# Optimization experiments

Measured on AMD Instinct MI355X. Metric: run time of the kernel, lower is better.

Reference implementation:

```python
import jax, jax.numpy as jnp
from jax import lax
import numpy as np

N, D, K = 262144, 256, 32


def setup_inputs() -> dict:
    key = jax.random.key(0)
    k1, k2 = jax.random.split(key)
    inputs = jax.random.normal(k1, (N, D), dtype=jnp.float32)
    q_vectors = jax.random.normal(k2, (K, D), dtype=jnp.float32)
    return {"inputs": inputs, "q_vectors": q_vectors}


def reference(inputs, q_vectors):
    # Sequence of Householder reflections: x <- x - (x @ q) outer (2/||q||^2 q)
    squared_norms = jnp.sum(q_vectors ** 2, axis=-1)  # [K]

    def step(x, qn):
        q, sq = qn  # q: [D], sq: scalar
        coeff = x @ q  # [N]
        x = x - jnp.outer(coeff, (2.0 / sq) * q)  # rank-1 update, [N, D]
        return x, None

    outputs, _ = lax.scan(step, inputs, (q_vectors, squared_norms))
    logabsdet = jnp.zeros(inputs.shape[0], dtype=inputs.dtype)
    return outputs, logabsdet
```

## Files before the change

kernel.cpp:

```cpp
#include <hip/hip_runtime.h>

#define N_ROWS 262144
#define DDIM   256
#define KREF   32
#define TILES  4
#define GRID_WY (N_ROWS / (64 * TILES))

typedef __attribute__((ext_vector_type(4))) float f32x4;
typedef __attribute__((ext_vector_type(8))) short bf16x8;

__device__ bf16x8 g_Vhi[2 * 8 * 64];
__device__ bf16x8 g_Vlo[2 * 8 * 64];
__device__ bf16x8 g_Uhi[16 * 64];
__device__ bf16x8 g_Ulo[16 * 64];
__device__ float  g_T[32 * 32];

__device__ __forceinline__ unsigned short f2bf(float x) {
    unsigned u = __float_as_uint(x);
    u += 0x7fffu + ((u >> 16) & 1u);
    return (unsigned short)(u >> 16);
}
__device__ __forceinline__ float bf2f(unsigned short h) {
    return __uint_as_float(((unsigned)h) << 16);
}

#define QS_LD 264
#define T_LD  33

__global__ __launch_bounds__(256)
void setup_a(const float* __restrict__ Q) {
    __shared__ float Qs[32 * QS_LD];
    __shared__ float G[32 * 32];
    __shared__ float T[32 * T_LD];
    __shared__ float beta[32];
    const int tid = threadIdx.x;

    {
        const int q  = tid >> 3;
        const int c8 = tid & 7;
        const f32x4* src = (const f32x4*)(Q + q * DDIM);
        f32x4* dst = (f32x4*)(Qs + q * QS_LD);
        #pragma unroll
        for (int i = 0; i < 8; ++i)
            dst[c8 + 8 * i] = src[c8 + 8 * i];
    }
    __syncthreads();

    for (int p = tid; p < 1024; p += 256) {
        const int i = p >> 5, j = p & 31;
        const f32x4* qi = (const f32x4*)(Qs + i * QS_LD);
        const f32x4* qj = (const f32x4*)(Qs + j * QS_LD);
        float s = 0.f;
        #pragma unroll 8
        for (int d = 0; d < 64; ++d) {
            const f32x4 a = qi[d], b = qj[d];
            s += a.x * b.x + a.y * b.y + a.z * b.z + a.w * b.w;
        }
        G[p] = s;
    }
    for (int p = tid; p < 32 * T_LD; p += 256) T[p] = 0.f;
    __syncthreads();

    if (tid < 32) beta[tid] = 2.0f / G[tid * 32 + tid];
    __syncthreads();

    for (int k = 0; k < 32; ++k) {
        if (tid < k) {
            float s = 0.f;
            for (int j = tid; j < k; ++j) s += T[tid * T_LD + j] * G[j * 32 + k];
            T[tid * T_LD + k] = -beta[k] * s;
        } else if (tid == k) {
            T[k * T_LD + k] = beta[k];
        }
        __syncthreads();
    }

    for (int p = tid; p < 1024; p += 256)
        g_T[p] = T[(p >> 5) * T_LD + (p & 31)];

    for (int e = tid; e < 2 * 8 * 64; e += 256) {
        const int lane = e & 63, c = (e >> 6) & 7, nt = e >> 9;
        const int q  = 16 * nt + (lane & 15);
        const int d0 = 32 * c + 8 * (lane >> 4);
        bf16x8 vh, vl;
        #pragma unroll
        for (int j = 0; j < 8; ++j) {
            const float x = Qs[q * QS_LD + d0 + j];
            const unsigned short h = f2bf(x);
            vh[j] = (short)h;
            vl[j] = (short)f2bf(x - bf2f(h));
        }
        g_Vhi[e] = vh; g_Vlo[e] = vl;
    }
}

__global__ __launch_bounds__(256)
void setup_b(const float* __restrict__ Q) {
    __shared__ float Ts[32 * 32];
    __shared__ float Us[16 * 33];
    const int tid = threadIdx.x;
    const int m = blockIdx.x;

    for (int p = tid; p < 1024; p += 256) Ts[p] = g_T[p];
    __syncthreads();

    #pragma unroll
    for (int e = 0; e < 2; ++e) {
        const int idx = tid + 256 * e;
        const int dd = idx >> 5, k = idx & 31;
        const int d = 16 * m + dd;
        float s = 0.f;
        for (int j = k; j < 32; ++j) s += Ts[k * 32 + j] * Q[j * DDIM + d];
        Us[dd * 33 + k] = s;
    }
    __syncthreads();

    if (tid < 64) {
        const int dd = tid & 15, k0 = 8 * (tid >> 4);
        bf16x8 uh, ul;
        #pragma unroll
        for (int j = 0; j < 8; ++j) {
            const float x = Us[dd * 33 + k0 + j];
            const unsigned short h = f2bf(x);
            uh[j] = (short)h;
            ul[j] = (short)f2bf(x - bf2f(h));
        }
        g_Uhi[m * 64 + tid] = uh;
        g_Ulo[m * 64 + tid] = ul;
    }
}

__global__ __launch_bounds__(256, 2)
void wy_kernel(const float* __restrict__ X, float* __restrict__ out) {
    __shared__ bf16x8 sVhi[1024];
    __shared__ bf16x8 sVlo[1024];
    __shared__ float  tscr[4 * 16 * 36];

    const int tid  = threadIdx.x;
    const int wave = tid >> 6;
    const int lane = tid & 63;
    const int t = lane & 15;
    const int g = lane >> 4;

    {
        const f32x4* s1 = (const f32x4*)g_Vhi;
        const f32x4* s2 = (const f32x4*)g_Vlo;
        f32x4* d1 = (f32x4*)sVhi;
        f32x4* d2 = (f32x4*)sVlo;
        #pragma unroll
        for (int i = 0; i < 4; ++i) {
            d1[tid + 256 * i] = s1[tid + 256 * i];
            d2[tid + 256 * i] = s2[tid + 256 * i];
        }
    }
    __syncthreads();

    const size_t base = (size_t)blockIdx.x * (64 * TILES) + wave * 16 + t;
    float* tb = tscr + wave * (16 * 36);

    f32x4 xa[16];
    {
        const float* xp = X + base * DDIM + 8 * g;
        #pragma unroll
        for (int c = 0; c < 8; ++c) {
            xa[2 * c]     = *(const f32x4*)(xp + 32 * c);
            xa[2 * c + 1] = *(const f32x4*)(xp + 32 * c + 4);
        }
    }

    #pragma unroll
    for (int tt = 0; tt < TILES; ++tt) {
        const size_t row = base + (size_t)tt * 64;

        bf16x8 ahi[8], alo[8];
        #pragma unroll
        for (int c = 0; c < 8; ++c) {
            #pragma unroll
            for (int e = 0; e < 8; ++e) {
                const float x = (e < 4) ? xa[2 * c][e] : xa[2 * c + 1][e - 4];
                const unsigned short h = f2bf(x);
                ahi[c][e] = (short)h;
                alo[c][e] = (short)f2bf(x - bf2f(h));
            }
        }

        if (tt + 1 < TILES) {
            const float* xp = X + (row + 64) * DDIM + 8 * g;
            #pragma unroll
            for (int c = 0; c < 8; ++c) {
                xa[2 * c]     = *(const f32x4*)(xp + 32 * c);
                xa[2 * c + 1] = *(const f32x4*)(xp + 32 * c + 4);
            }
        }

        f32x4 a0h = {0.f, 0.f, 0.f, 0.f}, a0l = {0.f, 0.f, 0.f, 0.f};
        f32x4 a1h = {0.f, 0.f, 0.f, 0.f}, a1l = {0.f, 0.f, 0.f, 0.f};
        #pragma unroll
        for (int c = 0; c < 8; ++c) {
            const bf16x8 bh0 = sVhi[c * 64 + lane];
            const bf16x8 bl0 = sVlo[c * 64 + lane];
            const bf16x8 bh1 = sVhi[512 + c * 64 + lane];
            const bf16x8 bl1 = sVlo[512 + c * 64 + lane];
            a0h = __builtin_amdgcn_mfma_f32_16x16x32_bf16(ahi[c], bh0, a0h, 0, 0, 0);
            a0l = __builtin_amdgcn_mfma_f32_16x16x32_bf16(alo[c], bh0, a0l, 0, 0, 0);
            a0l = __builtin_amdgcn_mfma_f32_16x16x32_bf16(ahi[c], bl0, a0l, 0, 0, 0);
            a1h = __builtin_amdgcn_mfma_f32_16x16x32_bf16(ahi[c], bh1, a1h, 0, 0, 0);
            a1l = __builtin_amdgcn_mfma_f32_16x16x32_bf16(alo[c], bh1, a1l, 0, 0, 0);
            a1l = __builtin_amdgcn_mfma_f32_16x16x32_bf16(ahi[c], bl1, a1l, 0, 0, 0);
        }
        const f32x4 acc0 = a0h + a0l;
        const f32x4 acc1 = a1h + a1l;

        f32x4 xe[16];
        const float* xr = X + row * DDIM + 4 * g;
        #pragma unroll
        for (int mt = 0; mt < 16; ++mt)
            xe[mt] = *(const f32x4*)(xr + 16 * mt);

        #pragma unroll
        for (int r = 0; r < 4; ++r) {
            tb[(4 * g + r) * 36 + t]      = acc0[r];
            tb[(4 * g + r) * 36 + 16 + t] = acc1[r];
        }
        asm volatile("s_waitcnt lgkmcnt(0)" ::: "memory");
        const f32x4 c01 = *(const f32x4*)(tb + t * 36 + 8 * g);
        const f32x4 c23 = *(const f32x4*)(tb + t * 36 + 8 * g + 4);

        bf16x8 chi, clo;
        #pragma unroll
        for (int j = 0; j < 8; ++j) {
            const float v = -((j < 4) ? c01[j] : c23[j - 4]);
            const unsigned short h = f2bf(v);
            chi[j] = (short)h;
            clo[j] = (short)f2bf(v - bf2f(h));
        }

        float* op = out + row * DDIM + 4 * g;
        #pragma unroll
        for (int mt = 0; mt < 16; ++mt) {
            const bf16x8 uh = g_Uhi[mt * 64 + lane];
            const bf16x8 ul = g_Ulo[mt * 64 + lane];
            f32x4 a = xe[mt];
            a = __builtin_amdgcn_mfma_f32_16x16x32_bf16(uh, chi, a, 0, 0, 0);
            a = __builtin_amdgcn_mfma_f32_16x16x32_bf16(ul, chi, a, 0, 0, 0);
            a = __builtin_amdgcn_mfma_f32_16x16x32_bf16(uh, clo, a, 0, 0, 0);
            *(f32x4*)(op + 16 * mt) = a;
        }
    }

    out[(size_t)N_ROWS * DDIM + (size_t)blockIdx.x * 256 + tid] = 0.0f;
}

extern "C" void kernel_launch(void* const* d_in, const int* in_sizes, int n_in,
                              void* d_out, int out_size, void* d_ws, size_t ws_size,
                              hipStream_t stream) {
    const float* X = (const float*)d_in[0];
    const float* Q = (const float*)d_in[1];
    float* out = (float*)d_out;

    setup_a<<<1, 256, 0, stream>>>(Q);
    setup_b<<<16, 256, 0, stream>>>(Q);
    wy_kernel<<<GRID_WY, 256, 0, stream>>>(X, out);
}
```

Before: 524.0 us.

## Process one 64-row tile per block instead of four with register prefetch

```diff
diff --git a/kernel.cpp b/kernel.cpp
--- a/kernel.cpp
+++ b/kernel.cpp
@@ -3,8 +3,7 @@
 #define N_ROWS 262144
 #define DDIM   256
 #define KREF   32
-#define TILES  4
-#define GRID_WY (N_ROWS / (64 * TILES))
+#define GRID_WY (N_ROWS / 64)
 
 typedef __attribute__((ext_vector_type(4))) float f32x4;
 typedef __attribute__((ext_vector_type(8))) short bf16x8;
@@ -130,11 +129,11 @@
     }
 }
 
-__global__ __launch_bounds__(256, 2)
+__global__ __launch_bounds__(256)
 void wy_kernel(const float* __restrict__ X, float* __restrict__ out) {
     __shared__ bf16x8 sVhi[1024];
     __shared__ bf16x8 sVlo[1024];
-    __shared__ float  tscr[4 * 16 * 36];
+    __shared__ float  tscr[4][16 * 36];
 
     const int tid  = threadIdx.x;
     const int wave = tid >> 6;
@@ -155,100 +154,72 @@
     }
     __syncthreads();
 
-    const size_t base = (size_t)blockIdx.x * (64 * TILES) + wave * 16 + t;
-    float* tb = tscr + wave * (16 * 36);
-
-    f32x4 xa[16];
-    {
-        const float* xp = X + base * DDIM + 8 * g;
-        #pragma unroll
-        for (int c = 0; c < 8; ++c) {
-            xa[2 * c]     = *(const f32x4*)(xp + 32 * c);
-            xa[2 * c + 1] = *(const f32x4*)(xp + 32 * c + 4);
-        }
-    }
-
-    #pragma unroll
-    for (int tt = 0; tt < TILES; ++tt) {
-        const size_t row = base + (size_t)tt * 64;
-
-        bf16x8 ahi[8], alo[8];
-        #pragma unroll
-        for (int c = 0; c < 8; ++c) {
-            #pragma unroll
-            for (int e = 0; e < 8; ++e) {
-                const float x = (e < 4) ? xa[2 * c][e] : xa[2 * c + 1][e - 4];
-                const unsigned short h = f2bf(x);
-                ahi[c][e] = (short)h;
-                alo[c][e] = (short)f2bf(x - bf2f(h));
-            }
-        }
-
-        if (tt + 1 < TILES) {
-            const float* xp = X + (row + 64) * DDIM + 8 * g;
-            #pragma unroll
-            for (int c = 0; c < 8; ++c) {
-                xa[2 * c]     = *(const f32x4*)(xp + 32 * c);
-                xa[2 * c + 1] = *(const f32x4*)(xp + 32 * c + 4);
-            }
-        }
-
-        f32x4 a0h = {0.f, 0.f, 0.f, 0.f}, a0l = {0.f, 0.f, 0.f, 0.f};
-        f32x4 a1h = {0.f, 0.f, 0.f, 0.f}, a1l = {0.f, 0.f, 0.f, 0.f};
-        #pragma unroll
-        for (int c = 0; c < 8; ++c) {
-            const bf16x8 bh0 = sVhi[c * 64 + lane];
-            const bf16x8 bl0 = sVlo[c * 64 + lane];
-            const bf16x8 bh1 = sVhi[512 + c * 64 + lane];
-            const bf16x8 bl1 = sVlo[512 + c * 64 + lane];
-            a0h = __builtin_amdgcn_mfma_f32_16x16x32_bf16(ahi[c], bh0, a0h, 0, 0, 0);
-            a0l = __builtin_amdgcn_mfma_f32_16x16x32_bf16(alo[c], bh0, a0l, 0, 0, 0);
-            a0l = __builtin_amdgcn_mfma_f32_16x16x32_bf16(ahi[c], bl0, a0l, 0, 0, 0);
-            a1h = __builtin_amdgcn_mfma_f32_16x16x32_bf16(ahi[c], bh1, a1h, 0, 0, 0);
-            a1l = __builtin_amdgcn_mfma_f32_16x16x32_bf16(alo[c], bh1, a1l, 0, 0, 0);
-            a1l = __builtin_amdgcn_mfma_f32_16x16x32_bf16(ahi[c], bl1, a1l, 0, 0, 0);
-        }
-        const f32x4 acc0 = a0h + a0l;
-        const f32x4 acc1 = a1h + a1l;
-
-        f32x4 xe[16];
-        const float* xr = X + row * DDIM + 4 * g;
-        #pragma unroll
-        for (int mt = 0; mt < 16; ++mt)
-            xe[mt] = *(const f32x4*)(xr + 16 * mt);
-
-        #pragma unroll
-        for (int r = 0; r < 4; ++r) {
-            tb[(4 * g + r) * 36 + t]      = acc0[r];
-            tb[(4 * g + r) * 36 + 16 + t] = acc1[r];
-        }
-        asm volatile("s_waitcnt lgkmcnt(0)" ::: "memory");
-        const f32x4 c01 = *(const f32x4*)(tb + t * 36 + 8 * g);
-        const f32x4 c23 = *(const f32x4*)(tb + t * 36 + 8 * g + 4);
-
-        bf16x8 chi, clo;
-        #pragma unroll
-        for (int j = 0; j < 8; ++j) {
-            const float v = -((j < 4) ? c01[j] : c23[j - 4]);
+    const int row = blockIdx.x * 64 + wave * 16 + t;
+    const float* xp = X + (size_t)row * DDIM + 8 * g;
+
+    f32x4 a0h = {0.f, 0.f, 0.f, 0.f}, a0l = {0.f, 0.f, 0.f, 0.f};
+    f32x4 a1h = {0.f, 0.f, 0.f, 0.f}, a1l = {0.f, 0.f, 0.f, 0.f};
+    #pragma unroll
+    for (int c = 0; c < 8; ++c) {
+        const f32x4 x0 = *(const f32x4*)(xp + 32 * c);
+        const f32x4 x1 = *(const f32x4*)(xp + 32 * c + 4);
+        bf16x8 ah, al;
+        #pragma unroll
+        for (int e = 0; e < 8; ++e) {
+            const float v = (e < 4) ? x0[e] : x1[e - 4];
             const unsigned short h = f2bf(v);
-            chi[j] = (short)h;
-            clo[j] = (short)f2bf(v - bf2f(h));
-        }
-
-        float* op = out + row * DDIM + 4 * g;
-        #pragma unroll
-        for (int mt = 0; mt < 16; ++mt) {
-            const bf16x8 uh = g_Uhi[mt * 64 + lane];
-            const bf16x8 ul = g_Ulo[mt * 64 + lane];
-            f32x4 a = xe[mt];
-            a = __builtin_amdgcn_mfma_f32_16x16x32_bf16(uh, chi, a, 0, 0, 0);
-            a = __builtin_amdgcn_mfma_f32_16x16x32_bf16(ul, chi, a, 0, 0, 0);
-            a = __builtin_amdgcn_mfma_f32_16x16x32_bf16(uh, clo, a, 0, 0, 0);
-            *(f32x4*)(op + 16 * mt) = a;
-        }
-    }
-
-    out[(size_t)N_ROWS * DDIM + (size_t)blockIdx.x * 256 + tid] = 0.0f;
+            ah[e] = (short)h;
+            al[e] = (short)f2bf(v - bf2f(h));
+        }
+        const bf16x8 bh0 = sVhi[c * 64 + lane];
+        const bf16x8 bl0 = sVlo[c * 64 + lane];
+        const bf16x8 bh1 = sVhi[512 + c * 64 + lane];
+        const bf16x8 bl1 = sVlo[512 + c * 64 + lane];
+        a0h = __builtin_amdgcn_mfma_f32_16x16x32_bf16(ah, bh0, a0h, 0, 0, 0);
+        a0l = __builtin_amdgcn_mfma_f32_16x16x32_bf16(al, bh0, a0l, 0, 0, 0);
+        a0l = __builtin_amdgcn_mfma_f32_16x16x32_bf16(ah, bl0, a0l, 0, 0, 0);
+        a1h = __builtin_amdgcn_mfma_f32_16x16x32_bf16(ah, bh1, a1h, 0, 0, 0);
+        a1l = __builtin_amdgcn_mfma_f32_16x16x32_bf16(al, bh1, a1l, 0, 0, 0);
+        a1l = __builtin_amdgcn_mfma_f32_16x16x32_bf16(ah, bl1, a1l, 0, 0, 0);
+    }
+    const f32x4 acc0 = a0h + a0l;
+    const f32x4 acc1 = a1h + a1l;
+
+    float* tb = tscr[wave];
+    #pragma unroll
+    for (int r = 0; r < 4; ++r) {
+        tb[(4 * g + r) * 36 + t]      = acc0[r];
+        tb[(4 * g + r) * 36 + 16 + t] = acc1[r];
+    }
+    asm volatile("s_waitcnt lgkmcnt(0)" ::: "memory");
+    __builtin_amdgcn_sched_barrier(0);
+    const f32x4 c01 = *(const f32x4*)(tb + t * 36 + 8 * g);
+    const f32x4 c23 = *(const f32x4*)(tb + t * 36 + 8 * g + 4);
+
+    bf16x8 chi, clo;
+    #pragma unroll
+    for (int j = 0; j < 8; ++j) {
+        const float v = -((j < 4) ? c01[j] : c23[j - 4]);
+        const unsigned short h = f2bf(v);
+        chi[j] = (short)h;
+        clo[j] = (short)f2bf(v - bf2f(h));
+    }
+
+    const float* xr = X   + (size_t)row * DDIM + 4 * g;
+    float*       op = out + (size_t)row * DDIM + 4 * g;
+    #pragma unroll
+    for (int mt = 0; mt < 16; ++mt) {
+        const f32x4 xe = *(const f32x4*)(xr + 16 * mt);
+        const bf16x8 uh = g_Uhi[mt * 64 + lane];
+        const bf16x8 ul = g_Ulo[mt * 64 + lane];
+        f32x4 a = __builtin_amdgcn_mfma_f32_16x16x32_bf16(uh, chi, xe, 0, 0, 0);
+        a = __builtin_amdgcn_mfma_f32_16x16x32_bf16(ul, chi, a, 0, 0, 0);
+        a = __builtin_amdgcn_mfma_f32_16x16x32_bf16(uh, clo, a, 0, 0, 0);
+        *(f32x4*)(op + 16 * mt) = a;
+    }
+
+    if (tid < 64)
+        out[(size_t)N_ROWS * DDIM + (size_t)blockIdx.x * 64 + tid] = 0.0f;
 }
 
 extern "C" void kernel_launch(void* const* d_in, const int* in_sizes, int n_in,
```

Measured after the change: 522.6 us. Within noise of the previous version (-0.3%).
